# Optimization experiments

Measured on AMD Instinct MI355X. Metric: run time of the kernel, lower is better.

Reference implementation:

```python
import jax, jax.numpy as jnp
import numpy as np

SCOPE = 63
IN_CHANNELS = 512
DAMP = 0.12
STD = 8.0


def _mexican_hat(scope, damping, std):
    # Ricker wavelet, centered, shape (1, 1, scope)
    x = jnp.arange(scope, dtype=jnp.float32) - (scope - 1) / 2.0
    norm = damping * (2.0 / (jnp.sqrt(3.0 * std) * np.pi ** 0.25))
    k = norm * (1.0 - (x / std) ** 2) * jnp.exp(-(x ** 2) / (2.0 * std ** 2))
    return k[None, None, :]


def setup_inputs() -> dict:
    key = jax.random.key(0)
    activations = jax.random.normal(key, (32, IN_CHANNELS, 56, 56), dtype=jnp.float32)
    inhibition_filter = _mexican_hat(SCOPE, DAMP, STD)
    return {"activations": activations, "inhibition_filter": inhibition_filter}


def _pad_roll(k, in_channels, scope):
    # zero-pad filter to length in_channels, then roll center to index 0 side
    pad_left = (in_channels - scope) // 2
    pad_right = in_channels - scope - pad_left
    padded = jnp.concatenate(
        [jnp.zeros((pad_left,), k.dtype), k, jnp.zeros((pad_right,), k.dtype)]
    )
    return jnp.roll(padded, in_channels // 2 + 1)


def reference(activations, inhibition_filter):
    C = activations.shape[1]
    kernel = _pad_roll(inhibition_filter[0, 0], C, SCOPE)  # (C,)
    # Circulant Toeplitz matrix: tpl[i] = roll(kernel, i), i.e. tpl[i, j] = kernel[(j - i) % C]
    idx = (jnp.arange(C)[None, :] - jnp.arange(C)[:, None]) % C
    tpl = kernel[idx]  # (C, C)
    # Original: [B, HW, C] @ [C, C] contracting input channel (first tpl axis)
    return jnp.einsum('bchw,cd->bdhw', activations, tpl)
```

## Files before the change

### kernel.cpp

```cpp
#include <hip/hip_runtime.h>
#include <hip/hip_bf16.h>
#include <cstddef>


#define NC    512
#define HW    3136
#define NT    32
#define NTILE (HW / NT)
#define NB    32
#define TPB   256

typedef __attribute__((ext_vector_type(8)))  short bf16x8;
typedef __attribute__((ext_vector_type(4)))  float f32x4;
typedef __attribute__((ext_vector_type(16))) float f32x16;

__device__ __forceinline__ short f2bf(float f) {
    union { __hip_bfloat16 h; short s; } u;
    u.h = __float2bfloat16(f);
    return u.s;
}

__device__ __forceinline__ int swzf(int hw) {
    return (((hw & 7) ^ (hw >> 3)) << 4);
}

__global__ __launch_bounds__(TPB, 4)
void toeplitz_mfma32_kernel(const float* __restrict__ act,
                            const float* __restrict__ filt,
                            float* __restrict__ out) {
    __shared__ __align__(16) unsigned short xs[NT * NC];

    const int tid  = threadIdx.x;
    const int wv   = tid >> 6;
    const int ln   = tid & 63;
    const int bx   = blockIdx.x;
    const int b    = bx / NTILE;
    const int tile = bx - b * NTILE;
    const int hw0  = tile * NT;

    const int r_a = ln & 31;
    const int k0  = (ln >> 5) * 8;
    bf16x8 af[6];
    #pragma unroll
    for (int m = 0; m < 6; ++m) {
        const int delta = 32 - 16 * m;
        #pragma unroll
        for (int i = 0; i < 8; ++i) {
            const int t = delta + 31 + r_a - (k0 + i);
            af[m][i] = (t >= 0 && t < 63) ? f2bf(filt[t]) : (short)0;
        }
    }

    {
        const float* gb = act + (size_t)b * NC * HW + hw0;
        const int g = ln >> 3;
        const int q = ln & 7;
        #pragma unroll
        for (int j = 0; j < 8; ++j) {
            const int r0 = wv * 128 + j * 16 + 2 * g;
            const f32x4 a0 = *reinterpret_cast<const f32x4*>(gb + (size_t)r0 * HW + 4 * q);
            const f32x4 a1 = *reinterpret_cast<const f32x4*>(gb + (size_t)(r0 + 1) * HW + 4 * q);
            #pragma unroll
            for (int t4 = 0; t4 < 4; ++t4) {
                const int hw = 4 * q + t4;
                const unsigned int pk = (unsigned int)(unsigned short)f2bf(a0[t4])
                                      | ((unsigned int)(unsigned short)f2bf(a1[t4]) << 16);
                const int byte = hw * (NC * 2) + ((r0 * 2) ^ swzf(hw));
                *reinterpret_cast<unsigned int*>(reinterpret_cast<char*>(xs) + byte) = pk;
            }
        }
    }
    __syncthreads();

    const int hwl  = ln & 31;
    const int rowbyte = hwl * (NC * 2);
    const int swzv    = swzf(hwl);
    const int kb      = (ln >> 5) * 16;

    #define BFRAG(c0) (*reinterpret_cast<const bf16x8*>(                      \
        reinterpret_cast<const char*>(xs) +                                   \
        (rowbyte + (((((c0) & (NC - 1)) * 2) + kb) ^ swzv))))

    bf16x8 w[12];
    {
        const int cbase = wv * 128 - 32;
        #pragma unroll
        for (int i = 0; i < 12; ++i)
            w[i] = BFRAG(cbase + 16 * i);
    }

    float* ob = out + (size_t)b * NC * HW + hw0 + hwl;
    const int rhalf = (ln >> 5) * 4;

    #pragma unroll
    for (int j = 0; j < 4; ++j) {
        const int d0 = wv * 128 + j * 32;
        f32x16 acc;
        #pragma unroll
        for (int r = 0; r < 16; ++r) acc[r] = 0.0f;
        #pragma unroll
        for (int m = 0; m < 6; ++m)
            acc = __builtin_amdgcn_mfma_f32_32x32x16_bf16(af[m], w[2 * j + m], acc, 0, 0, 0);
        #pragma unroll
        for (int r = 0; r < 16; ++r) {
            const int row = d0 + (r & 3) + 8 * (r >> 2) + rhalf;
            __builtin_nontemporal_store(acc[r], ob + (size_t)row * HW);
        }
    }
    #undef BFRAG
}

extern "C" void kernel_launch(void* const* d_in, const int* in_sizes, int n_in,
                              void* d_out, int out_size, void* d_ws, size_t ws_size,
                              hipStream_t stream) {
    const float* act  = (const float*)d_in[0];
    const float* filt = (const float*)d_in[1];
    float* out = (float*)d_out;
    dim3 grid(NB * NTILE);
    dim3 block(TPB);
    hipLaunchKernelGGL(toeplitz_mfma32_kernel, grid, block, 0, stream,
                       act, filt, out);
}
```

Before: 68.81 us.

## Process two HW tiles per block with double-buffered LDS prefetch

Each block now handles two consecutive 32-column tiles. The second tile's global loads are issued into registers before the first tile's MFMA and store phase, then written to a second LDS buffer. The aim is to overlap global load latency with compute and stores and to amortise the filter-fragment setup across two tiles. In exchange the grid is halved, LDS use doubles, more registers are needed, and launch bounds drop to 2 blocks per SM, which may reduce occupancy on a kernel that is memory bound.

```diff
diff --git a/kernel.cpp b/kernel.cpp
--- a/kernel.cpp
+++ b/kernel.cpp
@@ -6,9 +6,11 @@
 #define NC    512
 #define HW    3136
 #define NT    32
-#define NTILE (HW / NT)
+#define NTILE 98
 #define NB    32
 #define TPB   256
+#define TPW   2
+#define NPAIR (NTILE / TPW)
 
 typedef __attribute__((ext_vector_type(8)))  short bf16x8;
 typedef __attribute__((ext_vector_type(4)))  float f32x4;
@@ -24,19 +26,45 @@
     return (((hw & 7) ^ (hw >> 3)) << 4);
 }
 
-__global__ __launch_bounds__(TPB, 4)
-void toeplitz_mfma32_kernel(const float* __restrict__ act,
-                            const float* __restrict__ filt,
-                            float* __restrict__ out) {
-    __shared__ __align__(16) unsigned short xs[NT * NC];
+__device__ __forceinline__ void load_tile(const float* __restrict__ gb,
+                                          int wv, int g, int q, f32x4 (&r)[16]) {
+    #pragma unroll
+    for (int j = 0; j < 8; ++j) {
+        const int r0 = wv * 128 + j * 16 + 2 * g;
+        r[2 * j]     = *reinterpret_cast<const f32x4*>(gb + (size_t)r0 * HW + 4 * q);
+        r[2 * j + 1] = *reinterpret_cast<const f32x4*>(gb + (size_t)(r0 + 1) * HW + 4 * q);
+    }
+}
 
-    const int tid  = threadIdx.x;
-    const int wv   = tid >> 6;
-    const int ln   = tid & 63;
-    const int bx   = blockIdx.x;
-    const int b    = bx / NTILE;
-    const int tile = bx - b * NTILE;
-    const int hw0  = tile * NT;
+__device__ __forceinline__ void store_tile(unsigned short* __restrict__ dst,
+                                           int wv, int g, int q, const f32x4 (&r)[16]) {
+    #pragma unroll
+    for (int j = 0; j < 8; ++j) {
+        const int r0 = wv * 128 + j * 16 + 2 * g;
+        #pragma unroll
+        for (int t4 = 0; t4 < 4; ++t4) {
+            const int hw = 4 * q + t4;
+            const unsigned int pk = (unsigned int)(unsigned short)f2bf(r[2 * j][t4])
+                                  | ((unsigned int)(unsigned short)f2bf(r[2 * j + 1][t4]) << 16);
+            const int byte = hw * (NC * 2) + ((r0 * 2) ^ swzf(hw));
+            *reinterpret_cast<unsigned int*>(reinterpret_cast<char*>(dst) + byte) = pk;
+        }
+    }
+}
+
+__global__ __launch_bounds__(TPB, 2)
+void toeplitz_pipe_kernel(const float* __restrict__ act,
+                          const float* __restrict__ filt,
+                          float* __restrict__ out) {
+    __shared__ __align__(16) unsigned short xs[2][NT * NC];
+
+    const int tid = threadIdx.x;
+    const int wv  = tid >> 6;
+    const int ln  = tid & 63;
+    const int bx  = blockIdx.x;
+    const int b   = bx / NPAIR;
+    const int pr  = bx - b * NPAIR;
+    const int t0  = pr * TPW;
 
     const int r_a = ln & 31;
     const int k0  = (ln >> 5) * 8;
@@ -51,63 +79,59 @@
         }
     }
 
+    const int g = ln >> 3;
+    const int q = ln & 7;
+    const float* gbase = act + (size_t)b * NC * HW;
+
     {
-        const float* gb = act + (size_t)b * NC * HW + hw0;
-        const int g = ln >> 3;
-        const int q = ln & 7;
-        #pragma unroll
-        for (int j = 0; j < 8; ++j) {
-            const int r0 = wv * 128 + j * 16 + 2 * g;
-            const f32x4 a0 = *reinterpret_cast<const f32x4*>(gb + (size_t)r0 * HW + 4 * q);
-            const f32x4 a1 = *reinterpret_cast<const f32x4*>(gb + (size_t)(r0 + 1) * HW + 4 * q);
-            #pragma unroll
-            for (int t4 = 0; t4 < 4; ++t4) {
-                const int hw = 4 * q + t4;
-                const unsigned int pk = (unsigned int)(unsigned short)f2bf(a0[t4])
-                                      | ((unsigned int)(unsigned short)f2bf(a1[t4]) << 16);
-                const int byte = hw * (NC * 2) + ((r0 * 2) ^ swzf(hw));
-                *reinterpret_cast<unsigned int*>(reinterpret_cast<char*>(xs) + byte) = pk;
-            }
-        }
+        f32x4 R[16];
+        load_tile(gbase + (size_t)t0 * NT, wv, g, q, R);
+        store_tile(xs[0], wv, g, q, R);
     }
     __syncthreads();
 
-    const int hwl  = ln & 31;
+    const int hwl     = ln & 31;
     const int rowbyte = hwl * (NC * 2);
     const int swzv    = swzf(hwl);
-    const int kb      = (ln >> 5) * 16;
-
-    #define BFRAG(c0) (*reinterpret_cast<const bf16x8*>(                      \
-        reinterpret_cast<const char*>(xs) +                                   \
-        (rowbyte + (((((c0) & (NC - 1)) * 2) + kb) ^ swzv))))
-
-    bf16x8 w[12];
-    {
-        const int cbase = wv * 128 - 32;
-        #pragma unroll
-        for (int i = 0; i < 12; ++i)
-            w[i] = BFRAG(cbase + 16 * i);
-    }
-
-    float* ob = out + (size_t)b * NC * HW + hw0 + hwl;
-    const int rhalf = (ln >> 5) * 4;
+    const int kbv     = (ln >> 5) * 16;
+    const int rhalf   = (ln >> 5) * 4;
+    const int cbase   = wv * 128 - 32;
 
     #pragma unroll
-    for (int j = 0; j < 4; ++j) {
-        const int d0 = wv * 128 + j * 32;
-        f32x16 acc;
+    for (int i = 0; i < TPW; ++i) {
+        f32x4 Rn[16];
+        if (i + 1 < TPW)
+            load_tile(gbase + (size_t)(t0 + i + 1) * NT, wv, g, q, Rn);
+
+        const char* xb = reinterpret_cast<const char*>(xs[i & 1]);
+        bf16x8 w[12];
         #pragma unroll
-        for (int r = 0; r < 16; ++r) acc[r] = 0.0f;
+        for (int u = 0; u < 12; ++u) {
+            const int c0 = (cbase + 16 * u) & (NC - 1);
+            w[u] = *reinterpret_cast<const bf16x8*>(xb + rowbyte + (((c0 * 2) + kbv) ^ swzv));
+        }
+        float* ob = out + (size_t)b * NC * HW + (size_t)(t0 + i) * NT + hwl;
         #pragma unroll
-        for (int m = 0; m < 6; ++m)
-            acc = __builtin_amdgcn_mfma_f32_32x32x16_bf16(af[m], w[2 * j + m], acc, 0, 0, 0);
-        #pragma unroll
-        for (int r = 0; r < 16; ++r) {
-            const int row = d0 + (r & 3) + 8 * (r >> 2) + rhalf;
-            __builtin_nontemporal_store(acc[r], ob + (size_t)row * HW);
+        for (int j = 0; j < 4; ++j) {
+            const int d0 = wv * 128 + j * 32;
+            f32x16 acc;
+            #pragma unroll
+            for (int r = 0; r < 16; ++r) acc[r] = 0.0f;
+            #pragma unroll
+            for (int m = 0; m < 6; ++m)
+                acc = __builtin_amdgcn_mfma_f32_32x32x16_bf16(af[m], w[2 * j + m], acc, 0, 0, 0);
+            #pragma unroll
+            for (int r = 0; r < 16; ++r) {
+                const int row = d0 + (r & 3) + 8 * (r >> 2) + rhalf;
+                __builtin_nontemporal_store(acc[r], ob + (size_t)row * HW);
+            }
+        }
+
+        if (i + 1 < TPW) {
+            store_tile(xs[(i + 1) & 1], wv, g, q, Rn);
+            __syncthreads();
         }
     }
-    #undef BFRAG
 }
 
 extern "C" void kernel_launch(void* const* d_in, const int* in_sizes, int n_in,
@@ -116,8 +140,8 @@
     const float* act  = (const float*)d_in[0];
     const float* filt = (const float*)d_in[1];
     float* out = (float*)d_out;
-    dim3 grid(NB * NTILE);
+    dim3 grid(NB * NPAIR);
     dim3 block(TPB);
-    hipLaunchKernelGGL(toeplitz_mfma32_kernel, grid, block, 0, stream,
+    hipLaunchKernelGGL(toeplitz_pipe_kernel, grid, block, 0, stream,
                        act, filt, out);
 }
```

New measurement: 71.91 us. 1.05x slower.

## Load B fragments directly from global memory, dropping LDS staging

Applied to the files above, without the earlier changes.

Drops the shared-memory transpose and staging of the activation tile. Each lane now loads its MFMA B fragment straight from global memory, reading 8 strided rows of 32 contiguous floats each, and converts them to bf16 in registers. The fragment loads are interleaved with the four output tiles so that loads overlap MFMA work. This removes the LDS writes, the barrier and the LDS reads, and frees occupancy from shared memory. The cost is narrow 4-byte global loads instead of 16-byte vector loads, and wave-boundary rows (the wrap halo) are loaded twice by adjacent waves.

```diff
diff --git a/kernel.cpp b/kernel.cpp
--- a/kernel.cpp
+++ b/kernel.cpp
@@ -6,12 +6,11 @@
 #define NC    512
 #define HW    3136
 #define NT    32
-#define NTILE (HW / NT)
+#define NTILE 98
 #define NB    32
 #define TPB   256
 
 typedef __attribute__((ext_vector_type(8)))  short bf16x8;
-typedef __attribute__((ext_vector_type(4)))  float f32x4;
 typedef __attribute__((ext_vector_type(16))) float f32x16;
 
 __device__ __forceinline__ short f2bf(float f) {
@@ -20,23 +19,29 @@
     return u.s;
 }
 
-__device__ __forceinline__ int swzf(int hw) {
-    return (((hw & 7) ^ (hw >> 3)) << 4);
+__device__ __forceinline__ bf16x8 load_frag(const float* __restrict__ base,
+                                            int row0) {
+    float f[8];
+    #pragma unroll
+    for (int i = 0; i < 8; ++i)
+        f[i] = base[(size_t)(row0 + i) * HW];
+    bf16x8 w;
+    #pragma unroll
+    for (int i = 0; i < 8; ++i)
+        w[i] = f2bf(f[i]);
+    return w;
 }
 
 __global__ __launch_bounds__(TPB, 4)
-void toeplitz_mfma32_kernel(const float* __restrict__ act,
+void toeplitz_direct_kernel(const float* __restrict__ act,
                             const float* __restrict__ filt,
                             float* __restrict__ out) {
-    __shared__ __align__(16) unsigned short xs[NT * NC];
-
-    const int tid  = threadIdx.x;
-    const int wv   = tid >> 6;
-    const int ln   = tid & 63;
-    const int bx   = blockIdx.x;
-    const int b    = bx / NTILE;
-    const int tile = bx - b * NTILE;
-    const int hw0  = tile * NT;
+    const int tid = threadIdx.x;
+    const int wv  = tid >> 6;
+    const int ln  = tid & 63;
+    const int bx  = blockIdx.x;
+    const int b   = bx / NTILE;
+    const int hw0 = (bx - b * NTILE) * NT;
 
     const int r_a = ln & 31;
     const int k0  = (ln >> 5) * 8;
@@ -51,63 +56,55 @@
         }
     }
 
-    {
-        const float* gb = act + (size_t)b * NC * HW + hw0;
-        const int g = ln >> 3;
-        const int q = ln & 7;
-        #pragma unroll
-        for (int j = 0; j < 8; ++j) {
-            const int r0 = wv * 128 + j * 16 + 2 * g;
-            const f32x4 a0 = *reinterpret_cast<const f32x4*>(gb + (size_t)r0 * HW + 4 * q);
-            const f32x4 a1 = *reinterpret_cast<const f32x4*>(gb + (size_t)(r0 + 1) * HW + 4 * q);
-            #pragma unroll
-            for (int t4 = 0; t4 < 4; ++t4) {
-                const int hw = 4 * q + t4;
-                const unsigned int pk = (unsigned int)(unsigned short)f2bf(a0[t4])
-                                      | ((unsigned int)(unsigned short)f2bf(a1[t4]) << 16);
-                const int byte = hw * (NC * 2) + ((r0 * 2) ^ swzf(hw));
-                *reinterpret_cast<unsigned int*>(reinterpret_cast<char*>(xs) + byte) = pk;
-            }
-        }
-    }
-    __syncthreads();
+    const int col = ln & 31;
+    const int kh  = ln >> 5;
+    const float* base = act + (size_t)b * NC * HW + hw0 + col
+                            + (size_t)kh * 8 * HW;
+    float* ob = out + (size_t)b * NC * HW + hw0 + col;
+    const int rhalf = kh * 4;
+    const int cb    = wv * 128 - 32;
 
-    const int hwl  = ln & 31;
-    const int rowbyte = hwl * (NC * 2);
-    const int swzv    = swzf(hwl);
-    const int kb      = (ln >> 5) * 16;
+    #define ROW0(u) ((cb + 16 * (u) + NC) & (NC - 1))
 
-    #define BFRAG(c0) (*reinterpret_cast<const bf16x8*>(                      \
-        reinterpret_cast<const char*>(xs) +                                   \
-        (rowbyte + (((((c0) & (NC - 1)) * 2) + kb) ^ swzv))))
-
-    bf16x8 w[12];
-    {
-        const int cbase = wv * 128 - 32;
-        #pragma unroll
-        for (int i = 0; i < 12; ++i)
-            w[i] = BFRAG(cbase + 16 * i);
+    #define DO_TILE(j, wa, wb, wc, wd, we, wf)                                 \
+    {                                                                          \
+        const int d0 = wv * 128 + (j) * 32;                                    \
+        f32x16 acc;                                                            \
+        _Pragma("unroll") for (int r = 0; r < 16; ++r) acc[r] = 0.0f;          \
+        acc = __builtin_amdgcn_mfma_f32_32x32x16_bf16(af[0], wa, acc, 0, 0, 0);\
+        acc = __builtin_amdgcn_mfma_f32_32x32x16_bf16(af[1], wb, acc, 0, 0, 0);\
+        acc = __builtin_amdgcn_mfma_f32_32x32x16_bf16(af[2], wc, acc, 0, 0, 0);\
+        acc = __builtin_amdgcn_mfma_f32_32x32x16_bf16(af[3], wd, acc, 0, 0, 0);\
+        acc = __builtin_amdgcn_mfma_f32_32x32x16_bf16(af[4], we, acc, 0, 0, 0);\
+        acc = __builtin_amdgcn_mfma_f32_32x32x16_bf16(af[5], wf, acc, 0, 0, 0);\
+        _Pragma("unroll") for (int r = 0; r < 16; ++r) {                       \
+            const int row = d0 + (r & 3) + 8 * (r >> 2) + rhalf;               \
+            __builtin_nontemporal_store(acc[r], ob + (size_t)row * HW);        \
+        }                                                                      \
     }
 
-    float* ob = out + (size_t)b * NC * HW + hw0 + hwl;
-    const int rhalf = (ln >> 5) * 4;
+    bf16x8 w0 = load_frag(base, ROW0(0));
+    bf16x8 w1 = load_frag(base, ROW0(1));
+    bf16x8 w2 = load_frag(base, ROW0(2));
+    bf16x8 w3 = load_frag(base, ROW0(3));
+    bf16x8 w4 = load_frag(base, ROW0(4));
+    bf16x8 w5 = load_frag(base, ROW0(5));
+    DO_TILE(0, w0, w1, w2, w3, w4, w5)
 
-    #pragma unroll
-    for (int j = 0; j < 4; ++j) {
-        const int d0 = wv * 128 + j * 32;
-        f32x16 acc;
-        #pragma unroll
-        for (int r = 0; r < 16; ++r) acc[r] = 0.0f;
-        #pragma unroll
-        for (int m = 0; m < 6; ++m)
-            acc = __builtin_amdgcn_mfma_f32_32x32x16_bf16(af[m], w[2 * j + m], acc, 0, 0, 0);
-        #pragma unroll
-        for (int r = 0; r < 16; ++r) {
-            const int row = d0 + (r & 3) + 8 * (r >> 2) + rhalf;
-            __builtin_nontemporal_store(acc[r], ob + (size_t)row * HW);
-        }
-    }
-    #undef BFRAG
+    bf16x8 w6 = load_frag(base, ROW0(6));
+    bf16x8 w7 = load_frag(base, ROW0(7));
+    DO_TILE(1, w2, w3, w4, w5, w6, w7)
+
+    bf16x8 w8 = load_frag(base, ROW0(8));
+    bf16x8 w9 = load_frag(base, ROW0(9));
+    DO_TILE(2, w4, w5, w6, w7, w8, w9)
+
+    bf16x8 wA = load_frag(base, ROW0(10));
+    bf16x8 wB = load_frag(base, ROW0(11));
+    DO_TILE(3, w6, w7, w8, w9, wA, wB)
+
+    #undef DO_TILE
+    #undef ROW0
 }
 
 extern "C" void kernel_launch(void* const* d_in, const int* in_sizes, int n_in,
@@ -118,6 +115,6 @@
     float* out = (float*)d_out;
     dim3 grid(NB * NTILE);
     dim3 block(TPB);
-    hipLaunchKernelGGL(toeplitz_mfma32_kernel, grid, block, 0, stream,
+    hipLaunchKernelGGL(toeplitz_direct_kernel, grid, block, 0, stream,
                        act, filt, out);
 }
```

New measurement: 79.92 us. +16.1%, slower.
